# Kernel optimization log

Measured on AMD Instinct MI355X. Metric: run time of the kernel, lower is better.

## Reference

```python
import jax, jax.numpy as jnp
import numpy as np
import math

E = 512      # embed_dim
H = 8        # num_heads
D = E // H   # head_embed_dim
B = 1
S = 4096

def setup_inputs() -> dict:
    key = jax.random.key(0)
    ks = jax.random.split(key, 9)
    s = 1.0 / math.sqrt(E)
    return {
        "Q": jax.random.normal(ks[0], (B, S, E), dtype=jnp.float32),
        "K": jax.random.normal(ks[1], (B, S, E), dtype=jnp.float32),
        "V": jax.random.normal(ks[2], (B, S, E), dtype=jnp.float32),
        "W_qk": jax.random.uniform(ks[3], (E, E), jnp.float32, -s, s),
        "b_qk": jax.random.uniform(ks[4], (E,), jnp.float32, -s, s),
        "W_v": jax.random.uniform(ks[5], (E, E), jnp.float32, -s, s),
        "b_v": jax.random.uniform(ks[6], (E,), jnp.float32, -s, s),
        "W_out": jax.random.uniform(ks[7], (E, E), jnp.float32, -s, s),
        "b_out": jax.random.uniform(ks[8], (E,), jnp.float32, -s, s),
    }

def reference(Q, K, V, W_qk, b_qk, W_v, b_v, W_out, b_out):
    # shared qk projection (torch Linear: x @ W.T + b)
    q = Q @ W_qk.T + b_qk
    k = K @ W_qk.T + b_qk
    v = V @ W_v.T + b_v
    # NOTE: original uses .view(B, H, S, D) -- a pure reshape, no transpose
    q = q.reshape(B, H, S, D)
    k = k.reshape(B, H, S, D)
    v = v.reshape(B, H, S, D)
    scores = jnp.einsum("bhsd,bhtd->bhst", q, k) / math.sqrt(D)
    attn = jax.nn.softmax(scores, axis=-1)
    out = jnp.einsum("bhst,bhtd->bhsd", attn, v)
    out = out.reshape(B, S, E)  # matches .view merge
    return out @ W_out.T + b_out
```

## Files before the change

kernel.cpp:

```cpp
#include <hip/hip_runtime.h>
#include <hip/hip_bf16.h>
#include <math.h>

typedef __hip_bfloat16 hbf16;
typedef __attribute__((ext_vector_type(4))) float f32x4;
typedef __attribute__((ext_vector_type(8))) __bf16 bf16x8;
typedef __attribute__((ext_vector_type(4))) short short4v;

#define MFMA16(a, b, c) __builtin_amdgcn_mfma_f32_16x16x32_bf16((a), (b), (c), 0, 0, 0)

#if __has_builtin(__builtin_amdgcn_mfma_f32_16x16x16bf16_1k)
#define MFMA16K16(a, b, c) __builtin_amdgcn_mfma_f32_16x16x16bf16_1k((a), (b), (c), 0, 0, 0)
#else
__device__ __forceinline__ f32x4 mfma16k16_asm(short4v a, short4v b, f32x4 c) {
  asm("v_mfma_f32_16x16x16_bf16 %0, %1, %2, %0" : "+v"(c) : "v"(a), "v"(b));
  return c;
}
#define MFMA16K16(a, b, c) mfma16k16_asm((a), (b), (c))
#endif

__device__ __forceinline__ void gload_lds16(const hbf16* g, hbf16* l) {
  __builtin_amdgcn_global_load_lds(
      (const __attribute__((address_space(1))) void*)g,
      (__attribute__((address_space(3))) void*)l, 16, 0, 0);
}

__device__ __forceinline__ void cvt4(const float* __restrict__ s, hbf16* __restrict__ d, int i) {
  float4 v = reinterpret_cast<const float4*>(s)[i];
  union { hbf16 h[4]; uint2 u; } pk;
  pk.h[0] = __float2bfloat16(v.x);
  pk.h[1] = __float2bfloat16(v.y);
  pk.h[2] = __float2bfloat16(v.z);
  pk.h[3] = __float2bfloat16(v.w);
  reinterpret_cast<uint2*>(d)[i] = pk.u;
}

__global__ __launch_bounds__(256) void cvt_all_kernel(
    const float* __restrict__ Q, const float* __restrict__ K, const float* __restrict__ V,
    const float* __restrict__ Wqk, const float* __restrict__ Wv, const float* __restrict__ Wout,
    hbf16* __restrict__ Qb, hbf16* __restrict__ Kb, hbf16* __restrict__ Vb,
    hbf16* __restrict__ Wqkb, hbf16* __restrict__ Wvb, hbf16* __restrict__ Woutb,
    int n4big, int n4w) {
  int stride = gridDim.x * blockDim.x;
  for (int i = blockIdx.x * blockDim.x + threadIdx.x; i < n4big; i += stride) {
    cvt4(Q, Qb, i);
    cvt4(K, Kb, i);
    cvt4(V, Vb, i);
    if (i < n4w) {
      cvt4(Wqk, Wqkb, i);
      cvt4(Wv, Wvb, i);
      cvt4(Wout, Woutb, i);
    }
  }
}

__device__ __forceinline__ void gemm_core_128(
    const hbf16* __restrict__ A, const hbf16* __restrict__ B, int K, int bm, int bn,
    hbf16* Alds, hbf16* Blds, f32x4 (&acc)[4][4]) {
  const int tid = threadIdx.x;
  const int lane = tid & 63;
  const int wave = tid >> 6;
  const int wr = wave >> 1, wc = wave & 1;
  const int l15 = lane & 15, lg = lane >> 4;
  const hbf16* Abase = A + (size_t)bm * 128 * K;
  const hbf16* Bbase = B + (size_t)bn * 128 * K;
  for (int k0 = 0; k0 < K; k0 += 32) {
    if (k0) __syncthreads();
#pragma unroll
    for (int rr = 0; rr < 2; ++rr) {
      int chunk = rr * 256 + tid;
      int row = chunk >> 2;
      int c8 = (chunk & 3) << 3;
      gload_lds16(Abase + (size_t)row * K + k0 + c8, Alds + (rr * 4 + wave) * 512);
      gload_lds16(Bbase + (size_t)row * K + k0 + c8, Blds + (rr * 4 + wave) * 512);
    }
    __syncthreads();
    bf16x8 af[4], bfv[4];
#pragma unroll
    for (int m = 0; m < 4; ++m)
      af[m] = *reinterpret_cast<const bf16x8*>(&Alds[(wr * 64 + m * 16 + l15) * 32 + lg * 8]);
#pragma unroll
    for (int n = 0; n < 4; ++n)
      bfv[n] = *reinterpret_cast<const bf16x8*>(&Blds[(wc * 64 + n * 16 + l15) * 32 + lg * 8]);
#pragma unroll
    for (int m = 0; m < 4; ++m)
#pragma unroll
      for (int n = 0; n < 4; ++n)
        acc[m][n] = MFMA16(af[m], bfv[n], acc[m][n]);
  }
}

__global__ __launch_bounds__(256) void proj_fused_kernel(
    const hbf16* __restrict__ Qb, const hbf16* __restrict__ Kb, const hbf16* __restrict__ Vb,
    const hbf16* __restrict__ Wqk, const hbf16* __restrict__ Wv,
    const float* __restrict__ bqk, const float* __restrict__ bv,
    hbf16* __restrict__ qp, hbf16* __restrict__ kp, hbf16* __restrict__ vT) {
  __shared__ __align__(16) hbf16 Alds[128 * 32];
  __shared__ __align__(16) hbf16 Blds[128 * 32];
  const int z = blockIdx.y;
  const int lane = threadIdx.x & 63, wave = threadIdx.x >> 6;
  const int wr = wave >> 1, wc = wave & 1;
  const int l15 = lane & 15, lg = lane >> 4;

  f32x4 acc[4][4];
  const f32x4 zero = {0.f, 0.f, 0.f, 0.f};
#pragma unroll
  for (int m = 0; m < 4; ++m)
#pragma unroll
    for (int n = 0; n < 4; ++n) acc[m][n] = zero;

  if (z < 2) {
    const hbf16* A = z ? Kb : Qb;
    hbf16* outp = z ? kp : qp;
    const int bm = blockIdx.x & 31, bn = blockIdx.x >> 5;
    gemm_core_128(A, Wqk, 512, bm, bn, Alds, Blds, acc);
    const float qscale = z ? 1.0f : 0.125f * 1.4426950408889634f;
    const int row0 = bm * 128 + wr * 64;
    const int col0 = bn * 128 + wc * 64;
#pragma unroll
    for (int m = 0; m < 4; ++m) {
#pragma unroll
      for (int n = 0; n < 4; ++n) {
        const int col = col0 + n * 16 + l15;
        const float bsv = bqk[col];
#pragma unroll
        for (int j = 0; j < 4; ++j) {
          const int row = row0 + m * 16 + lg * 4 + j;
          outp[(size_t)row * 512 + col] = __float2bfloat16((acc[m][n][j] + bsv) * qscale);
        }
      }
    }
  } else {
    const int bm = blockIdx.x >> 5;
    const int bn = blockIdx.x & 31;
    gemm_core_128(Wv, Vb, 512, bm, bn, Alds, Blds, acc);
    const int row0 = bm * 128 + wr * 64;
    const int col0 = bn * 128 + wc * 64;
#pragma unroll
    for (int m = 0; m < 4; ++m) {
#pragma unroll
      for (int n = 0; n < 4; ++n) {
        const int col = col0 + n * 16 + l15;
#pragma unroll
        for (int j = 0; j < 4; ++j) {
          const int row = row0 + m * 16 + lg * 4 + j;
          const int h = col >> 9;
          const int p = ((col & 511) << 3) + (row >> 6);
          const int d = row & 63;
          vT[(size_t)h * 262144 + (size_t)d * 4096 + p] =
              __float2bfloat16(acc[m][n][j] + bv[row]);
        }
      }
    }
  }
}

__global__ __launch_bounds__(256) void out_gemm_kernel(
    const hbf16* __restrict__ A, const hbf16* __restrict__ B, const float* __restrict__ bias,
    float* __restrict__ out) {
  __shared__ __align__(16) hbf16 Alds[128 * 32];
  __shared__ __align__(16) hbf16 Blds[128 * 32];
  const int bm = blockIdx.x & 31, bn = blockIdx.x >> 5;
  f32x4 acc[4][4];
  const f32x4 zero = {0.f, 0.f, 0.f, 0.f};
#pragma unroll
  for (int m = 0; m < 4; ++m)
#pragma unroll
    for (int n = 0; n < 4; ++n) acc[m][n] = zero;

  gemm_core_128(A, B, 512, bm, bn, Alds, Blds, acc);

  const int lane = threadIdx.x & 63, wave = threadIdx.x >> 6;
  const int wr = wave >> 1, wc = wave & 1;
  const int l15 = lane & 15, lg = lane >> 4;
  const int row0 = bm * 128 + wr * 64;
  const int col0 = bn * 128 + wc * 64;
#pragma unroll
  for (int m = 0; m < 4; ++m) {
#pragma unroll
    for (int n = 0; n < 4; ++n) {
      const int col = col0 + n * 16 + l15;
      const float bsv = bias[col];
#pragma unroll
      for (int j = 0; j < 4; ++j) {
        const int row = row0 + m * 16 + lg * 4 + j;
        out[(size_t)row * 512 + col] = acc[m][n][j] + bsv;
      }
    }
  }
}

__device__ __forceinline__ void stage64(const hbf16* __restrict__ g, int gstride,
                                        hbf16* tile, int wave, int lane) {
#pragma unroll
  for (int ii = 0; ii < 2; ++ii) {
    const int i = wave * 2 + ii;
    const int row = i * 8 + (lane >> 3);
    const int ce = ((lane & 7) ^ (lane >> 3)) << 3;
    gload_lds16(g + (size_t)row * gstride + ce, tile + i * 512);
  }
}

template <bool DIRECT>
__global__ __launch_bounds__(256, 4) void attn_kernel4(
    const hbf16* __restrict__ qp, const hbf16* __restrict__ kp,
    const hbf16* __restrict__ vT, hbf16* __restrict__ ao,
    float* __restrict__ Opart, float* __restrict__ Lpart,
    int kv_per_split, int nwg) {
  const int lin = blockIdx.x + 32 * (blockIdx.y + 8 * blockIdx.z);
  const int chunk = nwg >> 3;
  const int swz = (lin & 7) * chunk + (lin >> 3);
  const int qt = swz & 31;
  const int h = (swz >> 5) & 7;
  const int split = swz >> 8;

  const hbf16* qh = qp + (size_t)h * 262144;
  const hbf16* kh = kp + (size_t)h * 262144;
  const hbf16* vh = vT + (size_t)h * 262144;

  const int lane = threadIdx.x & 63, wave = threadIdx.x >> 6;
  const int l15 = lane & 15, lg = lane >> 4;
  const int qrow0 = qt * 128 + wave * 32;
  const int kv0 = split * kv_per_split;
  const int nkt = kv_per_split >> 6;

  __shared__ __align__(16) hbf16 Kt[2][4096];
  __shared__ __align__(16) hbf16 Vt[2][4096];

  bf16x8 qf[2][2];
#pragma unroll
  for (int rb = 0; rb < 2; ++rb)
#pragma unroll
    for (int dc = 0; dc < 2; ++dc)
      qf[rb][dc] = *reinterpret_cast<const bf16x8*>(
          &qh[(size_t)(qrow0 + rb * 16 + l15) * 64 + dc * 32 + lg * 8]);

  float lsum[2] = {0.f, 0.f};
  f32x4 oaccT[2][4];
  const f32x4 zero = {0.f, 0.f, 0.f, 0.f};
#pragma unroll
  for (int rb = 0; rb < 2; ++rb)
#pragma unroll
    for (int db = 0; db < 4; ++db) oaccT[rb][db] = zero;

  stage64(kh + (size_t)kv0 * 64, 64, Kt[0], wave, lane);
  stage64(vh + kv0, 4096, Vt[0], wave, lane);
  __syncthreads();

  int cur = 0;
  for (int t = 0; t < nkt; ++t) {
    if (t + 1 < nkt) {
      const int kb = kv0 + (t + 1) * 64;
      stage64(kh + (size_t)kb * 64, 64, Kt[cur ^ 1], wave, lane);
      stage64(vh + kb, 4096, Vt[cur ^ 1], wave, lane);
    }
    const hbf16* Kc = Kt[cur];
    const hbf16* Vc = Vt[cur];

    f32x4 s[2][4];
#pragma unroll
    for (int rb = 0; rb < 2; ++rb)
#pragma unroll
      for (int cb = 0; cb < 4; ++cb) s[rb][cb] = zero;
#pragma unroll
    for (int cb = 0; cb < 4; ++cb) {
      const int krow = cb * 16 + l15;
      const int sw = l15 & 7;
#pragma unroll
      for (int dc = 0; dc < 2; ++dc) {
        bf16x8 kf = *reinterpret_cast<const bf16x8*>(
            &Kc[krow * 64 + (((dc * 4 + lg) ^ sw) << 3)]);
#pragma unroll
        for (int rb = 0; rb < 2; ++rb) s[rb][cb] = MFMA16(kf, qf[rb][dc], s[rb][cb]);
      }
    }

    short4v pb[2][4];
#pragma unroll
    for (int rb = 0; rb < 2; ++rb)
#pragma unroll
      for (int cb = 0; cb < 4; ++cb) {
        const float p0 = exp2f(s[rb][cb][0]);
        const float p1 = exp2f(s[rb][cb][1]);
        const float p2 = exp2f(s[rb][cb][2]);
        const float p3 = exp2f(s[rb][cb][3]);
        lsum[rb] += (p0 + p1) + (p2 + p3);
        union { hbf16 h[4]; short4v v; } pk;
        pk.h[0] = __float2bfloat16(p0);
        pk.h[1] = __float2bfloat16(p1);
        pk.h[2] = __float2bfloat16(p2);
        pk.h[3] = __float2bfloat16(p3);
        pb[rb][cb] = pk.v;
      }

#pragma unroll
    for (int db = 0; db < 4; ++db) {
      const int d = db * 16 + l15;
      const int swd = d & 7;
#pragma unroll
      for (int cb = 0; cb < 4; ++cb) {
        short4v vf = *reinterpret_cast<const short4v*>(
            &Vc[d * 64 + (((2 * cb + (lg >> 1)) ^ swd) << 3) + ((lg & 1) << 2)]);
#pragma unroll
        for (int rb = 0; rb < 2; ++rb)
          oaccT[rb][db] = MFMA16K16(vf, pb[rb][cb], oaccT[rb][db]);
      }
    }
    __syncthreads();
    cur ^= 1;
  }

#pragma unroll
  for (int rb = 0; rb < 2; ++rb) {
    lsum[rb] += __shfl_xor(lsum[rb], 16);
    lsum[rb] += __shfl_xor(lsum[rb], 32);
  }
  if (DIRECT) {
    hbf16* oh = ao + (size_t)h * 262144;
#pragma unroll
    for (int rb = 0; rb < 2; ++rb) {
      const float inv = 1.f / lsum[rb];
      const int row = qrow0 + rb * 16 + l15;
#pragma unroll
      for (int db = 0; db < 4; ++db) {
        union { hbf16 h[4]; uint2 u; } pk;
#pragma unroll
        for (int j = 0; j < 4; ++j) pk.h[j] = __float2bfloat16(oaccT[rb][db][j] * inv);
        *reinterpret_cast<uint2*>(&oh[(size_t)row * 64 + db * 16 + lg * 4]) = pk.u;
      }
    }
  } else {
    const size_t hrow0 = (size_t)split * 32768 + (size_t)h * 4096;
#pragma unroll
    for (int rb = 0; rb < 2; ++rb) {
      const int row = qrow0 + rb * 16 + l15;
#pragma unroll
      for (int db = 0; db < 4; ++db) {
        float4 v;
        v.x = oaccT[rb][db][0]; v.y = oaccT[rb][db][1];
        v.z = oaccT[rb][db][2]; v.w = oaccT[rb][db][3];
        *reinterpret_cast<float4*>(&Opart[(hrow0 + row) * 64 + db * 16 + lg * 4]) = v;
      }
      if (lg == 0) Lpart[hrow0 + row] = lsum[rb];
    }
  }
}

__global__ __launch_bounds__(256) void attn_combine_kernel(
    const float* __restrict__ Opart, const float* __restrict__ Lpart,
    hbf16* __restrict__ ao, int splits) {
  const int t = threadIdx.x;
  const int hrow = blockIdx.x * 64 + (t >> 2);
  const int d0 = (t & 3) * 16;
  float denom = 0.f;
  for (int s = 0; s < splits; ++s) denom += Lpart[s * 32768 + hrow];
  const float inv = 1.f / denom;
  float4 acc[4] = {};
  for (int s = 0; s < splits; ++s) {
    const float4* p = reinterpret_cast<const float4*>(
        Opart + ((size_t)s * 32768 + hrow) * 64 + d0);
#pragma unroll
    for (int i = 0; i < 4; ++i) {
      float4 v = p[i];
      acc[i].x += v.x; acc[i].y += v.y; acc[i].z += v.z; acc[i].w += v.w;
    }
  }
  union { hbf16 h[16]; uint4 u[2]; } pk;
#pragma unroll
  for (int i = 0; i < 4; ++i) {
    pk.h[i * 4 + 0] = __float2bfloat16(acc[i].x * inv);
    pk.h[i * 4 + 1] = __float2bfloat16(acc[i].y * inv);
    pk.h[i * 4 + 2] = __float2bfloat16(acc[i].z * inv);
    pk.h[i * 4 + 3] = __float2bfloat16(acc[i].w * inv);
  }
  uint4* dst = reinterpret_cast<uint4*>(ao + (size_t)hrow * 64 + d0);
  dst[0] = pk.u[0];
  dst[1] = pk.u[1];
}

extern "C" void kernel_launch(void* const* d_in, const int* in_sizes, int n_in,
                              void* d_out, int out_size, void* d_ws, size_t ws_size,
                              hipStream_t stream) {
  const float* Q = (const float*)d_in[0];
  const float* K = (const float*)d_in[1];
  const float* V = (const float*)d_in[2];
  const float* Wqk = (const float*)d_in[3];
  const float* bqk = (const float*)d_in[4];
  const float* Wv = (const float*)d_in[5];
  const float* bv = (const float*)d_in[6];
  const float* Wout = (const float*)d_in[7];
  const float* bout = (const float*)d_in[8];
  float* out = (float*)d_out;

  const size_t NE = (size_t)4096 * 512;
  const size_t WE = (size_t)512 * 512;
  hbf16* ws = (hbf16*)d_ws;
  hbf16* Qb = ws;
  hbf16* Kb = Qb + NE;
  hbf16* Vb = Kb + NE;
  hbf16* Wqkb = Vb + NE;
  hbf16* Wvb = Wqkb + WE;
  hbf16* Woutb = Wvb + WE;
  hbf16* qp = Woutb + WE;
  hbf16* kp = qp + NE;
  hbf16* vT = kp + NE;
  hbf16* ao = vT + NE;

  const size_t base_bytes = (((size_t)(7 * NE + 3 * WE) * 2) + 255) & ~(size_t)255;
  const size_t per_split_bytes = ((size_t)32768 * 64 + 32768) * 4;
  int splits = 1;
  if (ws_size >= base_bytes + 4 * per_split_bytes) splits = 4;
  else if (ws_size >= base_bytes + 2 * per_split_bytes) splits = 2;
  float* Opart = (float*)((char*)d_ws + base_bytes);
  float* Lpart = Opart + (size_t)splits * 32768 * 64;

  cvt_all_kernel<<<2048, 256, 0, stream>>>(Q, K, V, Wqk, Wv, Wout,
                                           Qb, Kb, Vb, Wqkb, Wvb, Woutb,
                                           (int)(NE / 4), (int)(WE / 4));
  proj_fused_kernel<<<dim3(128, 3), 256, 0, stream>>>(Qb, Kb, Vb, Wqkb, Wvb, bqk, bv,
                                                      qp, kp, vT);
  if (splits == 1) {
    attn_kernel4<true><<<dim3(32, 8, 1), 256, 0, stream>>>(
        qp, kp, vT, ao, nullptr, nullptr, 4096, 256);
  } else {
    attn_kernel4<false><<<dim3(32, 8, splits), 256, 0, stream>>>(
        qp, kp, vT, nullptr, Opart, Lpart, 4096 / splits, 256 * splits);
    attn_combine_kernel<<<512, 256, 0, stream>>>(Opart, Lpart, ao, splits);
  }
  out_gemm_kernel<<<128, 256, 0, stream>>>(ao, Woutb, bout, out);
}
```

Measured before the change: 181.6 us.

## Double-buffer projection GEMMs with 64x128 tiles and allow eight attention splits

The shared GEMM core is rewritten to load the next K-slice into a second LDS buffer while MFMAs run on the current one. This removes one barrier per iteration. Block tiles shrink from 128x128 to 64x128, with each wave owning a 64x32 strip, which doubles the block count for the projection and output GEMMs to fill more CUs. The attention split-K factor can now rise to 8 when the workspace allows, adding parallelism at the cost of more partial-result traffic in the combine kernel.

```diff
diff --git a/kernel.cpp b/kernel.cpp
--- a/kernel.cpp
+++ b/kernel.cpp
@@ -54,39 +54,53 @@
   }
 }
 
-__device__ __forceinline__ void gemm_core_128(
+__device__ __forceinline__ void stage_a64(const hbf16* __restrict__ A, int K, int bm, int k0,
+                                          hbf16* Alds, int wave, int lane) {
+  const int row = wave * 16 + (lane >> 2);
+  gload_lds16(A + (size_t)(bm * 64 + row) * K + k0 + (lane & 3) * 8, Alds + wave * 512);
+}
+__device__ __forceinline__ void stage_b128(const hbf16* __restrict__ B, int K, int bn, int k0,
+                                           hbf16* Blds, int wave, int lane) {
+#pragma unroll
+  for (int i = 0; i < 2; ++i) {
+    const int row = wave * 32 + i * 16 + (lane >> 2);
+    gload_lds16(B + (size_t)(bn * 128 + row) * K + k0 + (lane & 3) * 8,
+                Blds + wave * 1024 + i * 512);
+  }
+}
+
+__device__ __forceinline__ void gemm_core_2ph(
     const hbf16* __restrict__ A, const hbf16* __restrict__ B, int K, int bm, int bn,
-    hbf16* Alds, hbf16* Blds, f32x4 (&acc)[4][4]) {
+    hbf16* Alds , hbf16* Blds , f32x4 (&acc)[4][2]) {
   const int tid = threadIdx.x;
   const int lane = tid & 63;
   const int wave = tid >> 6;
-  const int wr = wave >> 1, wc = wave & 1;
   const int l15 = lane & 15, lg = lane >> 4;
-  const hbf16* Abase = A + (size_t)bm * 128 * K;
-  const hbf16* Bbase = B + (size_t)bn * 128 * K;
-  for (int k0 = 0; k0 < K; k0 += 32) {
-    if (k0) __syncthreads();
-#pragma unroll
-    for (int rr = 0; rr < 2; ++rr) {
-      int chunk = rr * 256 + tid;
-      int row = chunk >> 2;
-      int c8 = (chunk & 3) << 3;
-      gload_lds16(Abase + (size_t)row * K + k0 + c8, Alds + (rr * 4 + wave) * 512);
-      gload_lds16(Bbase + (size_t)row * K + k0 + c8, Blds + (rr * 4 + wave) * 512);
-    }
+  const int nt = K >> 5;
+  stage_a64(A, K, bm, 0, Alds, wave, lane);
+  stage_b128(B, K, bn, 0, Blds, wave, lane);
+  __syncthreads();
+  int cur = 0;
+  for (int t = 0; t < nt; ++t) {
+    if (t + 1 < nt) {
+      stage_a64(A, K, bm, (t + 1) * 32, Alds + (cur ^ 1) * 2048, wave, lane);
+      stage_b128(B, K, bn, (t + 1) * 32, Blds + (cur ^ 1) * 4096, wave, lane);
+    }
+    bf16x8 af[4], bfv[2];
+#pragma unroll
+    for (int m = 0; m < 4; ++m)
+      af[m] = *reinterpret_cast<const bf16x8*>(&Alds[cur * 2048 + (m * 16 + l15) * 32 + lg * 8]);
+#pragma unroll
+    for (int n = 0; n < 2; ++n)
+      bfv[n] = *reinterpret_cast<const bf16x8*>(
+          &Blds[cur * 4096 + (wave * 32 + n * 16 + l15) * 32 + lg * 8]);
+#pragma unroll
+    for (int m = 0; m < 4; ++m)
+#pragma unroll
+      for (int n = 0; n < 2; ++n)
+        acc[m][n] = MFMA16(af[m], bfv[n], acc[m][n]);
     __syncthreads();
-    bf16x8 af[4], bfv[4];
-#pragma unroll
-    for (int m = 0; m < 4; ++m)
-      af[m] = *reinterpret_cast<const bf16x8*>(&Alds[(wr * 64 + m * 16 + l15) * 32 + lg * 8]);
-#pragma unroll
-    for (int n = 0; n < 4; ++n)
-      bfv[n] = *reinterpret_cast<const bf16x8*>(&Blds[(wc * 64 + n * 16 + l15) * 32 + lg * 8]);
-#pragma unroll
-    for (int m = 0; m < 4; ++m)
-#pragma unroll
-      for (int n = 0; n < 4; ++n)
-        acc[m][n] = MFMA16(af[m], bfv[n], acc[m][n]);
+    cur ^= 1;
   }
 }
 
@@ -95,32 +109,31 @@
     const hbf16* __restrict__ Wqk, const hbf16* __restrict__ Wv,
     const float* __restrict__ bqk, const float* __restrict__ bv,
     hbf16* __restrict__ qp, hbf16* __restrict__ kp, hbf16* __restrict__ vT) {
-  __shared__ __align__(16) hbf16 Alds[128 * 32];
-  __shared__ __align__(16) hbf16 Blds[128 * 32];
+  __shared__ __align__(16) hbf16 Alds[2 * 2048];
+  __shared__ __align__(16) hbf16 Blds[2 * 4096];
   const int z = blockIdx.y;
   const int lane = threadIdx.x & 63, wave = threadIdx.x >> 6;
-  const int wr = wave >> 1, wc = wave & 1;
   const int l15 = lane & 15, lg = lane >> 4;
 
-  f32x4 acc[4][4];
+  f32x4 acc[4][2];
   const f32x4 zero = {0.f, 0.f, 0.f, 0.f};
 #pragma unroll
   for (int m = 0; m < 4; ++m)
 #pragma unroll
-    for (int n = 0; n < 4; ++n) acc[m][n] = zero;
+    for (int n = 0; n < 2; ++n) acc[m][n] = zero;
 
   if (z < 2) {
     const hbf16* A = z ? Kb : Qb;
     hbf16* outp = z ? kp : qp;
-    const int bm = blockIdx.x & 31, bn = blockIdx.x >> 5;
-    gemm_core_128(A, Wqk, 512, bm, bn, Alds, Blds, acc);
+    const int bm = blockIdx.x & 63, bn = blockIdx.x >> 6;
+    gemm_core_2ph(A, Wqk, 512, bm, bn, Alds, Blds, acc);
     const float qscale = z ? 1.0f : 0.125f * 1.4426950408889634f;
-    const int row0 = bm * 128 + wr * 64;
-    const int col0 = bn * 128 + wc * 64;
+    const int row0 = bm * 64;
+    const int col0 = bn * 128 + wave * 32;
 #pragma unroll
     for (int m = 0; m < 4; ++m) {
 #pragma unroll
-      for (int n = 0; n < 4; ++n) {
+      for (int n = 0; n < 2; ++n) {
         const int col = col0 + n * 16 + l15;
         const float bsv = bqk[col];
 #pragma unroll
@@ -133,13 +146,13 @@
   } else {
     const int bm = blockIdx.x >> 5;
     const int bn = blockIdx.x & 31;
-    gemm_core_128(Wv, Vb, 512, bm, bn, Alds, Blds, acc);
-    const int row0 = bm * 128 + wr * 64;
-    const int col0 = bn * 128 + wc * 64;
+    gemm_core_2ph(Wv, Vb, 512, bm, bn, Alds, Blds, acc);
+    const int row0 = bm * 64;
+    const int col0 = bn * 128 + wave * 32;
 #pragma unroll
     for (int m = 0; m < 4; ++m) {
 #pragma unroll
-      for (int n = 0; n < 4; ++n) {
+      for (int n = 0; n < 2; ++n) {
         const int col = col0 + n * 16 + l15;
 #pragma unroll
         for (int j = 0; j < 4; ++j) {
@@ -158,27 +171,26 @@
 __global__ __launch_bounds__(256) void out_gemm_kernel(
     const hbf16* __restrict__ A, const hbf16* __restrict__ B, const float* __restrict__ bias,
     float* __restrict__ out) {
-  __shared__ __align__(16) hbf16 Alds[128 * 32];
-  __shared__ __align__(16) hbf16 Blds[128 * 32];
-  const int bm = blockIdx.x & 31, bn = blockIdx.x >> 5;
-  f32x4 acc[4][4];
+  __shared__ __align__(16) hbf16 Alds[2 * 2048];
+  __shared__ __align__(16) hbf16 Blds[2 * 4096];
+  const int bm = blockIdx.x & 63, bn = blockIdx.x >> 6;
+  const int lane = threadIdx.x & 63, wave = threadIdx.x >> 6;
+  const int l15 = lane & 15, lg = lane >> 4;
+  f32x4 acc[4][2];
   const f32x4 zero = {0.f, 0.f, 0.f, 0.f};
 #pragma unroll
   for (int m = 0; m < 4; ++m)
 #pragma unroll
-    for (int n = 0; n < 4; ++n) acc[m][n] = zero;
-
-  gemm_core_128(A, B, 512, bm, bn, Alds, Blds, acc);
-
-  const int lane = threadIdx.x & 63, wave = threadIdx.x >> 6;
-  const int wr = wave >> 1, wc = wave & 1;
-  const int l15 = lane & 15, lg = lane >> 4;
-  const int row0 = bm * 128 + wr * 64;
-  const int col0 = bn * 128 + wc * 64;
+    for (int n = 0; n < 2; ++n) acc[m][n] = zero;
+
+  gemm_core_2ph(A, B, 512, bm, bn, Alds, Blds, acc);
+
+  const int row0 = bm * 64;
+  const int col0 = bn * 128 + wave * 32;
 #pragma unroll
   for (int m = 0; m < 4; ++m) {
 #pragma unroll
-    for (int n = 0; n < 4; ++n) {
+    for (int n = 0; n < 2; ++n) {
       const int col = col0 + n * 16 + l15;
       const float bsv = bias[col];
 #pragma unroll
@@ -409,7 +421,8 @@
   const size_t base_bytes = (((size_t)(7 * NE + 3 * WE) * 2) + 255) & ~(size_t)255;
   const size_t per_split_bytes = ((size_t)32768 * 64 + 32768) * 4;
   int splits = 1;
-  if (ws_size >= base_bytes + 4 * per_split_bytes) splits = 4;
+  if (ws_size >= base_bytes + 8 * per_split_bytes) splits = 8;
+  else if (ws_size >= base_bytes + 4 * per_split_bytes) splits = 4;
   else if (ws_size >= base_bytes + 2 * per_split_bytes) splits = 2;
   float* Opart = (float*)((char*)d_ws + base_bytes);
   float* Lpart = Opart + (size_t)splits * 32768 * 64;
@@ -417,7 +430,7 @@
   cvt_all_kernel<<<2048, 256, 0, stream>>>(Q, K, V, Wqk, Wv, Wout,
                                            Qb, Kb, Vb, Wqkb, Wvb, Woutb,
                                            (int)(NE / 4), (int)(WE / 4));
-  proj_fused_kernel<<<dim3(128, 3), 256, 0, stream>>>(Qb, Kb, Vb, Wqkb, Wvb, bqk, bv,
+  proj_fused_kernel<<<dim3(256, 3), 256, 0, stream>>>(Qb, Kb, Vb, Wqkb, Wvb, bqk, bv,
                                                       qp, kp, vT);
   if (splits == 1) {
     attn_kernel4<true><<<dim3(32, 8, 1), 256, 0, stream>>>(
@@ -427,5 +440,5 @@
         qp, kp, vT, nullptr, Opart, Lpart, 4096 / splits, 256 * splits);
     attn_combine_kernel<<<512, 256, 0, stream>>>(Opart, Lpart, ao, splits);
   }
-  out_gemm_kernel<<<128, 256, 0, stream>>>(ao, Woutb, bout, out);
-}
+  out_gemm_kernel<<<256, 256, 0, stream>>>(ao, Woutb, bout, out);
+}
```

Result: slower. 187.1 us (+3.0%).
